# Kernel optimization log

Hardware: AMD Instinct MI355X
Metric: run time of the kernel (lower is better)

The kernel has to match this reference:

```python
import jax, jax.numpy as jnp
import numpy as np

SCALE_FACTOR = 2
KERNEL_SIZE = SCALE_FACTOR + 1  # 3
SIGMA = 2.0
EPS = 1e-6


def _gaussian_kernel(k, sigma, dtype):
    ax = jnp.arange(k, dtype=jnp.float32) - (k - 1) / 2.0
    g = jnp.exp(-(ax[:, None] ** 2 + ax[None, :] ** 2) / (2.0 * sigma ** 2))
    return (g / g.sum()).astype(dtype)


def _smooth(img, kernel):
    # img: [B,H,W,C], kernel: [k,k]; depthwise gaussian blur, SAME padding
    C = img.shape[-1]
    k = kernel.shape[0]
    kern = jnp.tile(kernel[:, :, None, None], (1, 1, 1, C))  # HWIO, I=1 per group
    return jax.lax.conv_general_dilated(
        img, kern, window_strides=(1, 1), padding=[(k // 2, k // 2)] * 2,
        dimension_numbers=('NHWC', 'HWIO', 'NHWC'), feature_group_count=C)


def setup_inputs() -> dict:
    key = jax.random.key(0)
    k1, k2 = jax.random.split(key)
    B, N, C = 8, 3072, 256
    x = jax.random.normal(k1, (B, N, C), dtype=jnp.float32)
    loc = jax.random.uniform(k2, (B, N, 2), dtype=jnp.float32, minval=-1.0, maxval=1.0)
    return {"x": x, "loc": loc, "h": 64, "w": 48}


def reference(x, loc, h, w):
    # token2map(x, loc, [h*sf, w*sf], kernel_size=sf+1, sigma=2)
    H, W = int(h * SCALE_FACTOR), int(w * SCALE_FACTOR)
    B, N, C = x.shape
    loc = jnp.clip(loc, -1.0, 1.0)
    px = 0.5 * (loc[..., 0] + 1.0) * W - 0.5
    py = 0.5 * (loc[..., 1] + 1.0) * H - 0.5
    ix = jnp.clip(jnp.round(px).astype(jnp.int32), 0, W - 1)  # [B,N]
    iy = jnp.clip(jnp.round(py).astype(jnp.int32), 0, H - 1)
    idx = ix + iy * W + jnp.arange(B, dtype=jnp.int32)[:, None] * (H * W)  # [B,N]

    # scatter-add features and counts into the flat grid
    src = jnp.concatenate([x, jnp.ones((B, N, 1), x.dtype)], axis=-1).reshape(B * N, C + 1)
    acc = jnp.zeros((B * H * W, C + 1), x.dtype).at[idx.reshape(-1)].add(src)
    acc = acc.reshape(B, H, W, C + 1)
    feature = acc[..., :C]
    count = acc[..., C:]

    feature = feature / (count + EPS)
    mask = (count > 0).astype(x.dtype)
    feature = feature * mask

    # gaussian interpolation to fill empty cells
    kernel = _gaussian_kernel(KERNEL_SIZE, SIGMA, x.dtype)
    feat_s = _smooth(feature, kernel)
    mask_s = _smooth(mask, kernel)
    feat_s = feat_s / (mask_s + EPS)
    feat_s = feat_s * (mask_s > 0).astype(x.dtype)
    feature = feature + (1.0 - mask) * feat_s

    return jnp.transpose(feature, (0, 3, 1, 2))  # [B,C,H,W] to match torch layout
```

## Files before the change

kernel.cpp:

```cpp
#include <hip/hip_runtime.h>

#define B_  8
#define N_  3072
#define C_  256
#define H_  128
#define W_  96
#define HW_ (H_ * W_)
#define NC_ (B_ * HW_)
#define NT_ (B_ * N_)
#define EPSF 1e-6f

#define KW0 0.13080118f
#define KW1 0.11543166f
#define KW2 0.10186807f

#define CG_ 128
#define XT_ 32
#define XS_ 34
#define CPB 132
#define RY_ 2
#define NWG_ (B_ * (H_ / RY_) * 3 * 2)

#define OFF_ASTART 0
#define OFF_ACUR   (NC_ + 1)
#define OFF_BSUM   (2 * NC_ + 1)
#define OFF_BOFF   (2 * NC_ + 1 + 384)
#define OFF_TOKS   (2 * NC_ + 1 + 768)

__device__ __forceinline__ unsigned f2bf(float f) {
    const unsigned u = __float_as_uint(f);
    return (u + 0x7FFFu + ((u >> 16) & 1u)) >> 16;
}

__device__ __forceinline__ void token_cell(const float* __restrict__ loc, int token,
                                           int& b, int& ix, int& iy) {
    b = token / N_;
    const float lx = fminf(fmaxf(loc[2 * token + 0], -1.0f), 1.0f);
    const float ly = fminf(fmaxf(loc[2 * token + 1], -1.0f), 1.0f);
    const float px = 0.5f * (lx + 1.0f) * (float)W_ - 0.5f;
    const float py = 0.5f * (ly + 1.0f) * (float)H_ - 0.5f;
    ix = (int)rintf(px); ix = min(max(ix, 0), W_ - 1);
    iy = (int)rintf(py); iy = min(max(iy, 0), H_ - 1);
}

__global__ void count_k(const float* __restrict__ loc, unsigned* __restrict__ cnts) {
    const int token = blockIdx.x * 256 + threadIdx.x;
    int b, ix, iy;
    token_cell(loc, token, b, ix, iy);
    atomicAdd(&cnts[b * HW_ + iy * W_ + ix], 1u);
}

__global__ void scanA(const unsigned* __restrict__ cnts, unsigned* __restrict__ Bsum) {
    const int i = blockIdx.x * 256 + threadIdx.x;
    int c = (int)cnts[i];
    #pragma unroll
    for (int off = 32; off > 0; off >>= 1) c += __shfl_down(c, off, 64);
    __shared__ int s[4];
    if ((threadIdx.x & 63) == 0) s[threadIdx.x >> 6] = c;
    __syncthreads();
    if (threadIdx.x == 0) Bsum[blockIdx.x] = (unsigned)(s[0] + s[1] + s[2] + s[3]);
}

__global__ void scanB(const unsigned* __restrict__ Bsum, unsigned* __restrict__ Boff) {
    __shared__ unsigned s[512];
    const int t = threadIdx.x;
    const unsigned v = (t < 384) ? Bsum[t] : 0u;
    s[t] = v;
    __syncthreads();
    #pragma unroll
    for (int off = 1; off < 512; off <<= 1) {
        const unsigned a = (t >= off) ? s[t - off] : 0u;
        __syncthreads();
        s[t] += a;
        __syncthreads();
    }
    if (t < 384) Boff[t] = s[t] - v;
}

__global__ void scanC(const unsigned* __restrict__ Boff,
                      unsigned* __restrict__ Astart, unsigned* __restrict__ Acur) {
    __shared__ unsigned s[256];
    const int t = threadIdx.x;
    const int i = blockIdx.x * 256 + t;
    const unsigned v = Acur[i];
    s[t] = v;
    __syncthreads();
    #pragma unroll
    for (int off = 1; off < 256; off <<= 1) {
        const unsigned a = (t >= off) ? s[t - off] : 0u;
        __syncthreads();
        s[t] += a;
        __syncthreads();
    }
    const unsigned excl = s[t] - v + Boff[blockIdx.x];
    Astart[i] = excl;
    Acur[i]   = excl;
    if (i == 0) Astart[NC_] = NT_;
}

__global__ void fill_bins(const float* __restrict__ loc,
                          unsigned* __restrict__ Acur, unsigned* __restrict__ toks) {
    const int token = blockIdx.x * 256 + threadIdx.x;
    int b, ix, iy;
    token_cell(loc, token, b, ix, iy);
    const unsigned pos = atomicAdd(&Acur[b * HW_ + iy * W_ + ix], 1u);
    toks[pos] = ((unsigned)ix << 20) | (unsigned)token;
}

__device__ __forceinline__ void bf4_to_f32(const unsigned short* p, float* f) {
    const uint2 v = *(const uint2*)p;
    f[0] = __uint_as_float(v.x << 16);
    f[1] = __uint_as_float(v.x & 0xFFFF0000u);
    f[2] = __uint_as_float(v.y << 16);
    f[3] = __uint_as_float(v.y & 0xFFFF0000u);
}

__global__ __launch_bounds__(256) void fused_k(const float* __restrict__ xf,
        const unsigned* __restrict__ Astart, const unsigned* __restrict__ toks,
        float* __restrict__ out) {
    const int blk = (blockIdx.x & 7) * (NWG_ / 8) + (blockIdx.x >> 3);
    const int cg = blk & 1;
    const int t2 = blk >> 1;
    const int xt = t2 % 3;
    const int t3 = t2 / 3;
    const int yp = t3 & 63;
    const int b  = t3 >> 6;
    const int y0 = yp * RY_;
    const int xs = xt * XT_;
    const int lane = threadIdx.x & 63;
    const int wv = threadIdx.x >> 6;

    __shared__ __align__(16) unsigned short means[4 * XS_ * CPB];
    __shared__ unsigned long long cmask[4];
    __shared__ float coef[RY_][XT_][10];

    const int yg = y0 - 1 + wv;
    const bool inrow = ((unsigned)yg < (unsigned)H_);
    unsigned p0, p1;
    {
        unsigned a = 0u;
        if (inrow && lane < XS_ + 1) {
            int g = xs - 1 + lane;
            g = min(max(g, 0), W_);
            a = Astart[b * HW_ + yg * W_ + g];
        }
        const unsigned an = __shfl_down(a, 1, 64);
        const unsigned long long mask = __ballot(lane < XS_ && an > a);
        if (lane == 0) cmask[wv] = mask;
        p0 = __shfl(a, 0, 64);
        p1 = __shfl(a, XS_, 64);
    }

    {
        uint4* p4 = (uint4*)means;
        for (int i = threadIdx.x; i < 4 * XS_ * CPB / 8; i += 256)
            p4[i] = make_uint4(0u, 0u, 0u, 0u);
    }
    __syncthreads();

    if (wv == 0) {
        const int r  = lane >> 5;
        const int xl = lane & 31;
        const int xi = xl + 1;
        const unsigned long long cm0 = cmask[r], cm1 = cmask[r + 1],
                                 cm2 = cmask[r + 2];
        const float w0 = ((cm0 >> (xi - 1)) & 1ULL) ? KW2 : 0.0f;
        const float w1 = ((cm0 >> xi)       & 1ULL) ? KW1 : 0.0f;
        const float w2 = ((cm0 >> (xi + 1)) & 1ULL) ? KW2 : 0.0f;
        const float w3 = ((cm1 >> (xi - 1)) & 1ULL) ? KW1 : 0.0f;
        const float w5 = ((cm1 >> (xi + 1)) & 1ULL) ? KW1 : 0.0f;
        const float w6 = ((cm2 >> (xi - 1)) & 1ULL) ? KW2 : 0.0f;
        const float w7 = ((cm2 >> xi)       & 1ULL) ? KW1 : 0.0f;
        const float w8 = ((cm2 >> (xi + 1)) & 1ULL) ? KW2 : 0.0f;
        const bool ne  = (cm1 >> xi) & 1ULL;
        const float ms = ((w0 + w2) + (w6 + w8)) + ((w1 + w7) + (w3 + w5));
        const float inv = ne ? 0.0f : 1.0f / (ms + EPSF);
        coef[r][xl][0] = w0 * inv;
        coef[r][xl][1] = w1 * inv;
        coef[r][xl][2] = w2 * inv;
        coef[r][xl][3] = w3 * inv;
        coef[r][xl][4] = ne ? 1.0f : 0.0f;
        coef[r][xl][5] = w5 * inv;
        coef[r][xl][6] = w6 * inv;
        coef[r][xl][7] = w7 * inv;
        coef[r][xl][8] = w8 * inv;
    }

    if (inrow) {
        unsigned* msw = (unsigned*)(means + wv * XS_ * CPB);
        int cur_xi = -1;
        float acc0 = 0.0f, acc1 = 0.0f;
        unsigned cnt = 0u;
        for (unsigned p = p0; p < p1; p += 4) {
            unsigned vv[4]; float2 ff[4];
            #pragma unroll
            for (int j = 0; j < 4; ++j)
                if (p + j < p1) vv[j] = toks[p + j];
            #pragma unroll
            for (int j = 0; j < 4; ++j)
                if (p + j < p1)
                    ff[j] = *(const float2*)&xf[(size_t)(vv[j] & 0xFFFFFu) * C_
                                                + cg * CG_ + 2 * lane];
            #pragma unroll
            for (int j = 0; j < 4; ++j) {
                if (p + j >= p1) break;
                const int xi = (int)(vv[j] >> 20) - xs + 1;
                if (xi != cur_xi) {
                    if (cur_xi >= 0) {
                        const float rcp = 1.0f / ((float)cnt + EPSF);
                        msw[cur_xi * (CPB / 2) + lane] =
                            f2bf(acc0 * rcp) | (f2bf(acc1 * rcp) << 16);
                    }
                    acc0 = acc1 = 0.0f; cnt = 0u; cur_xi = xi;
                }
                acc0 += ff[j].x; acc1 += ff[j].y; ++cnt;
            }
        }
        if (cur_xi >= 0) {
            const float rcp = 1.0f / ((float)cnt + EPSF);
            msw[cur_xi * (CPB / 2) + lane] = f2bf(acc0 * rcp) | (f2bf(acc1 * rcp) << 16);
        }
    }
    __syncthreads();

    const int xl  = threadIdx.x & 31;
    const int sub = threadIdx.x >> 5;
    const int xi  = xl + 1;
    const int c0  = sub * 16;

    #pragma unroll
    for (int r = 0; r < RY_; ++r) {
        float c9[9];
        #pragma unroll
        for (int j = 0; j < 9; ++j) c9[j] = coef[r][xl][j];
        const unsigned short* M0 = means + (r    ) * XS_ * CPB;
        const unsigned short* M1 = means + (r + 1) * XS_ * CPB;
        const unsigned short* M2 = means + (r + 2) * XS_ * CPB;
        float* op = out + ((size_t)(b * C_ + cg * CG_ + c0)) * HW_
                        + (size_t)(y0 + r) * W_ + xs + xl;

        #pragma unroll
        for (int q = 0; q < 4; ++q) {
            const int cq = c0 + q * 4;
            const int im = (xi - 1) * CPB + cq;
            const int ic = (xi    ) * CPB + cq;
            const int ip = (xi + 1) * CPB + cq;
            float a0[4], a1[4], a2[4], b0[4], b1[4], b2[4], d0[4], d1[4], d2[4];
            bf4_to_f32(&M0[im], a0); bf4_to_f32(&M0[ic], a1); bf4_to_f32(&M0[ip], a2);
            bf4_to_f32(&M1[im], b0); bf4_to_f32(&M1[ic], b1); bf4_to_f32(&M1[ip], b2);
            bf4_to_f32(&M2[im], d0); bf4_to_f32(&M2[ic], d1); bf4_to_f32(&M2[ip], d2);
            #pragma unroll
            for (int k = 0; k < 4; ++k) {
                const float fs = c9[0]*a0[k] + c9[1]*a1[k] + c9[2]*a2[k]
                               + c9[3]*b0[k] + c9[4]*b1[k] + c9[5]*b2[k]
                               + c9[6]*d0[k] + c9[7]*d1[k] + c9[8]*d2[k];
                op[(size_t)(q * 4 + k) * HW_] = fs;
            }
        }
    }
}

extern "C" void kernel_launch(void* const* d_in, const int* in_sizes, int n_in,
                              void* d_out, int out_size, void* d_ws, size_t ws_size,
                              hipStream_t stream) {
    const float* x   = (const float*)d_in[0];
    const float* loc = (const float*)d_in[1];
    float* out = (float*)d_out;

    unsigned* W32 = (unsigned*)d_ws;
    unsigned* Astart = W32 + OFF_ASTART;
    unsigned* Acur   = W32 + OFF_ACUR;
    unsigned* Bsum   = W32 + OFF_BSUM;
    unsigned* Boff   = W32 + OFF_BOFF;
    unsigned* toks   = W32 + OFF_TOKS;

    hipMemsetAsync(Acur, 0, (size_t)NC_ * sizeof(unsigned), stream);

    count_k  <<<NT_ / 256, 256, 0, stream>>>(loc, Acur);
    scanA    <<<NC_ / 256, 256, 0, stream>>>(Acur, Bsum);
    scanB    <<<1, 512, 0, stream>>>(Bsum, Boff);
    scanC    <<<NC_ / 256, 256, 0, stream>>>(Boff, Astart, Acur);
    fill_bins<<<NT_ / 256, 256, 0, stream>>>(loc, Acur, toks);

    fused_k<<<NWG_, 256, 0, stream>>>(x, Astart, toks, out);
}
```

Measured before the change: 57.44 us.

## Store fp32 means in LDS with 64-channel groups and packed FMA stencil

Halves the channel group per workgroup (128 to 64), doubling the workgroup count, and keeps the per-cell means in LDS as fp32 instead of bf16. The 3x3 stencil now reads float4 pairs and accumulates with v_pk_fma_f32 over 8 channels per thread. This removes the bf16 pack/unpack ALU work and rounding error. In exchange each token's row of x is gathered by twice as many workgroups, with narrower scalar loads per lane.

```diff
diff --git a/kernel.cpp b/kernel.cpp
--- a/kernel.cpp
+++ b/kernel.cpp
@@ -14,12 +14,12 @@
 #define KW1 0.11543166f
 #define KW2 0.10186807f
 
-#define CG_ 128
+#define CG_ 64
 #define XT_ 32
 #define XS_ 34
-#define CPB 132
+#define CPB 68
 #define RY_ 2
-#define NWG_ (B_ * (H_ / RY_) * 3 * 2)
+#define NWG_ (B_ * (H_ / RY_) * 3 * 4)
 
 #define OFF_ASTART 0
 #define OFF_ACUR   (NC_ + 1)
@@ -27,9 +27,10 @@
 #define OFF_BOFF   (2 * NC_ + 1 + 384)
 #define OFF_TOKS   (2 * NC_ + 1 + 768)
 
-__device__ __forceinline__ unsigned f2bf(float f) {
-    const unsigned u = __float_as_uint(f);
-    return (u + 0x7FFFu + ((u >> 16) & 1u)) >> 16;
+__device__ __forceinline__ float2 pk_fma(float2 a, float2 b, float2 c) {
+    float2 d;
+    asm("v_pk_fma_f32 %0, %1, %2, %3" : "=v"(d) : "v"(a), "v"(b), "v"(c));
+    return d;
 }
 
 __device__ __forceinline__ void token_cell(const float* __restrict__ loc, int token,
@@ -107,20 +108,12 @@
     toks[pos] = ((unsigned)ix << 20) | (unsigned)token;
 }
 
-__device__ __forceinline__ void bf4_to_f32(const unsigned short* p, float* f) {
-    const uint2 v = *(const uint2*)p;
-    f[0] = __uint_as_float(v.x << 16);
-    f[1] = __uint_as_float(v.x & 0xFFFF0000u);
-    f[2] = __uint_as_float(v.y << 16);
-    f[3] = __uint_as_float(v.y & 0xFFFF0000u);
-}
-
 __global__ __launch_bounds__(256) void fused_k(const float* __restrict__ xf,
         const unsigned* __restrict__ Astart, const unsigned* __restrict__ toks,
         float* __restrict__ out) {
     const int blk = (blockIdx.x & 7) * (NWG_ / 8) + (blockIdx.x >> 3);
-    const int cg = blk & 1;
-    const int t2 = blk >> 1;
+    const int cg = blk & 3;
+    const int t2 = blk >> 2;
     const int xt = t2 % 3;
     const int t3 = t2 / 3;
     const int yp = t3 & 63;
@@ -130,7 +123,7 @@
     const int lane = threadIdx.x & 63;
     const int wv = threadIdx.x >> 6;
 
-    __shared__ __align__(16) unsigned short means[4 * XS_ * CPB];
+    __shared__ __align__(16) float means[4 * XS_ * CPB];
     __shared__ unsigned long long cmask[4];
     __shared__ float coef[RY_][XT_][10];
 
@@ -152,9 +145,9 @@
     }
 
     {
-        uint4* p4 = (uint4*)means;
-        for (int i = threadIdx.x; i < 4 * XS_ * CPB / 8; i += 256)
-            p4[i] = make_uint4(0u, 0u, 0u, 0u);
+        float4* p4 = (float4*)means;
+        for (int i = threadIdx.x; i < 4 * XS_ * CPB / 4; i += 256)
+            p4[i] = make_float4(0.f, 0.f, 0.f, 0.f);
     }
     __syncthreads();
 
@@ -187,76 +180,67 @@
     }
 
     if (inrow) {
-        unsigned* msw = (unsigned*)(means + wv * XS_ * CPB);
+        float* Ms = means + wv * XS_ * CPB;
         int cur_xi = -1;
-        float acc0 = 0.0f, acc1 = 0.0f;
+        float acc = 0.0f;
         unsigned cnt = 0u;
         for (unsigned p = p0; p < p1; p += 4) {
-            unsigned vv[4]; float2 ff[4];
+            unsigned vv[4]; float ff[4];
             #pragma unroll
             for (int j = 0; j < 4; ++j)
                 if (p + j < p1) vv[j] = toks[p + j];
             #pragma unroll
             for (int j = 0; j < 4; ++j)
                 if (p + j < p1)
-                    ff[j] = *(const float2*)&xf[(size_t)(vv[j] & 0xFFFFFu) * C_
-                                                + cg * CG_ + 2 * lane];
+                    ff[j] = xf[(size_t)(vv[j] & 0xFFFFFu) * C_ + cg * CG_ + lane];
             #pragma unroll
             for (int j = 0; j < 4; ++j) {
                 if (p + j >= p1) break;
                 const int xi = (int)(vv[j] >> 20) - xs + 1;
                 if (xi != cur_xi) {
-                    if (cur_xi >= 0) {
-                        const float rcp = 1.0f / ((float)cnt + EPSF);
-                        msw[cur_xi * (CPB / 2) + lane] =
-                            f2bf(acc0 * rcp) | (f2bf(acc1 * rcp) << 16);
-                    }
-                    acc0 = acc1 = 0.0f; cnt = 0u; cur_xi = xi;
+                    if (cur_xi >= 0)
+                        Ms[cur_xi * CPB + lane] = acc / ((float)cnt + EPSF);
+                    acc = 0.0f; cnt = 0u; cur_xi = xi;
                 }
-                acc0 += ff[j].x; acc1 += ff[j].y; ++cnt;
+                acc += ff[j]; ++cnt;
             }
         }
-        if (cur_xi >= 0) {
-            const float rcp = 1.0f / ((float)cnt + EPSF);
-            msw[cur_xi * (CPB / 2) + lane] = f2bf(acc0 * rcp) | (f2bf(acc1 * rcp) << 16);
-        }
+        if (cur_xi >= 0)
+            Ms[cur_xi * CPB + lane] = acc / ((float)cnt + EPSF);
     }
     __syncthreads();
 
     const int xl  = threadIdx.x & 31;
     const int sub = threadIdx.x >> 5;
     const int xi  = xl + 1;
-    const int c0  = sub * 16;
+    const int c0  = sub * 8;
 
     #pragma unroll
     for (int r = 0; r < RY_; ++r) {
         float c9[9];
         #pragma unroll
         for (int j = 0; j < 9; ++j) c9[j] = coef[r][xl][j];
-        const unsigned short* M0 = means + (r    ) * XS_ * CPB;
-        const unsigned short* M1 = means + (r + 1) * XS_ * CPB;
-        const unsigned short* M2 = means + (r + 2) * XS_ * CPB;
+
+        float2 a0 = make_float2(0.f, 0.f), a1 = a0, a2 = a0, a3 = a0;
+        #pragma unroll
+        for (int j = 0; j < 9; ++j) {
+            const int slot = r + j / 3;
+            const int col  = xi - 1 + j % 3;
+            const float* base = means + (slot * XS_ + col) * CPB + c0;
+            const float4 v0 = *(const float4*)base;
+            const float4 v1 = *(const float4*)(base + 4);
+            const float2 wp = make_float2(c9[j], c9[j]);
+            a0 = pk_fma(make_float2(v0.x, v0.y), wp, a0);
+            a1 = pk_fma(make_float2(v0.z, v0.w), wp, a1);
+            a2 = pk_fma(make_float2(v1.x, v1.y), wp, a2);
+            a3 = pk_fma(make_float2(v1.z, v1.w), wp, a3);
+        }
         float* op = out + ((size_t)(b * C_ + cg * CG_ + c0)) * HW_
                         + (size_t)(y0 + r) * W_ + xs + xl;
-
-        #pragma unroll
-        for (int q = 0; q < 4; ++q) {
-            const int cq = c0 + q * 4;
-            const int im = (xi - 1) * CPB + cq;
-            const int ic = (xi    ) * CPB + cq;
-            const int ip = (xi + 1) * CPB + cq;
-            float a0[4], a1[4], a2[4], b0[4], b1[4], b2[4], d0[4], d1[4], d2[4];
-            bf4_to_f32(&M0[im], a0); bf4_to_f32(&M0[ic], a1); bf4_to_f32(&M0[ip], a2);
-            bf4_to_f32(&M1[im], b0); bf4_to_f32(&M1[ic], b1); bf4_to_f32(&M1[ip], b2);
-            bf4_to_f32(&M2[im], d0); bf4_to_f32(&M2[ic], d1); bf4_to_f32(&M2[ip], d2);
-            #pragma unroll
-            for (int k = 0; k < 4; ++k) {
-                const float fs = c9[0]*a0[k] + c9[1]*a1[k] + c9[2]*a2[k]
-                               + c9[3]*b0[k] + c9[4]*b1[k] + c9[5]*b2[k]
-                               + c9[6]*d0[k] + c9[7]*d1[k] + c9[8]*d2[k];
-                op[(size_t)(q * 4 + k) * HW_] = fs;
-            }
-        }
+        op[(size_t)0 * HW_] = a0.x; op[(size_t)1 * HW_] = a0.y;
+        op[(size_t)2 * HW_] = a1.x; op[(size_t)3 * HW_] = a1.y;
+        op[(size_t)4 * HW_] = a2.x; op[(size_t)5 * HW_] = a2.y;
+        op[(size_t)6 * HW_] = a3.x; op[(size_t)7 * HW_] = a3.y;
     }
 }
 
```

Result: slower. 63.33 us (+10.3%).
